# Kernel optimization log

Hardware: AMD Instinct MI355X
Metric: run time of the kernel (lower is better)

Reference implementation:

```python
import jax, jax.numpy as jnp
import numpy as np

N, E, F_IN, C, L = 50000, 800000, 64, 128, 2  # nodes, edges, input feats, channels, EGNN layers


def layer_norm(x, g, b, eps=1e-5):
    m = jnp.mean(x, -1, keepdims=True)
    v = jnp.var(x, -1, keepdims=True)
    return (x - m) / jnp.sqrt(v + eps) * g + b


def setup_inputs() -> dict:
    key = jax.random.key(0)
    ks = jax.random.split(key, 12)
    w = lambda k, shape: jax.random.normal(k, shape, jnp.float32) * 0.02
    return dict(
        node_attr=jax.random.normal(ks[0], (N, F_IN), jnp.float32),
        xyz=jax.random.normal(ks[1], (N, 3), jnp.float32),
        src=jax.random.randint(ks[2], (E,), 0, N, jnp.int32),
        dst=jax.random.randint(ks[3], (E,), 0, N, jnp.int32),
        # initial_node_embedding: Linear -> LN -> GELU -> Linear -> LN -> GELU (dropout off in eval)
        W_in1=w(ks[4], (F_IN, C)), b_in1=jnp.zeros((C,), jnp.float32),
        g_in1=jnp.ones((C,), jnp.float32), be_in1=jnp.zeros((C,), jnp.float32),
        W_in2=w(ks[5], (C, C)), b_in2=jnp.zeros((C,), jnp.float32),
        g_in2=jnp.ones((C,), jnp.float32), be_in2=jnp.zeros((C,), jnp.float32),
        # per-layer EGNNConv params (edge_feat_size=0), stacked over L layers
        We1=w(ks[6], (L, 2 * C + 1, C)), be1=jnp.zeros((L, C), jnp.float32),
        We2=w(ks[7], (L, C, C)), be2=jnp.zeros((L, C), jnp.float32),
        Wn1=w(ks[8], (L, 2 * C, C)), bn1=jnp.zeros((L, C), jnp.float32),
        Wn2=w(ks[9], (L, C, C)), bn2=jnp.zeros((L, C), jnp.float32),
    )


def reference(node_attr, xyz, src, dst,
              W_in1, b_in1, g_in1, be_in1, W_in2, b_in2, g_in2, be_in2,
              We1, be1, We2, be2, Wn1, bn1, Wn2, bn2):
    # initial node embedding (eval mode: dropout = identity; do_dropout=False)
    h = jax.nn.gelu(layer_norm(node_attr @ W_in1 + b_in1, g_in1, be_in1), approximate=False)
    h = jax.nn.gelu(layer_norm(h @ W_in2 + b_in2, g_in2, be_in2), approximate=False)

    # geometry is recomputed from the SAME xyz every layer (GraphConv passes the
    # original coord_feat to each EGNNConv and discards the updated coords)
    x_diff = xyz[src] - xyz[dst]                        # [E, 3]
    radial = jnp.sum(x_diff * x_diff, -1, keepdims=True)  # [E, 1]

    for l in range(L):
        f = jnp.concatenate([h[src], h[dst], radial], -1)  # [E, 2C+1]
        msg = jax.nn.silu(f @ We1[l] + be1[l])
        msg = jax.nn.silu(msg @ We2[l] + be2[l])            # [E, C]
        h_neigh = jax.ops.segment_sum(msg, dst, num_segments=N)  # sum to destination
        h = jax.nn.silu(jnp.concatenate([h, h_neigh], -1) @ Wn1[l] + bn1[l]) @ Wn2[l] + bn2[l]
    return h
```

## Files before the change

kernel.cpp:

```cpp
#include <hip/hip_runtime.h>
#include <stdint.h>

#define NND 50000
#define NED 800000
#define CH  128

typedef unsigned short us;
typedef unsigned int u32;
using bf16x8 = __attribute__((ext_vector_type(8))) __bf16;
using f32x4  = __attribute__((ext_vector_type(4))) float;

static __device__ __forceinline__ us f2bfu(float f){
  __bf16 b = (__bf16)f;
  return __builtin_bit_cast(us, b);
}
static __device__ __forceinline__ float silu_f(float x){
  return __fdividef(x, 1.0f + __expf(-x));
}
static __device__ __forceinline__ f32x4 mfma16(bf16x8 a, bf16x8 b, f32x4 c){
  return __builtin_amdgcn_mfma_f32_16x16x32_bf16(a, b, c, 0, 0, 0);
}
static __device__ __forceinline__ bf16x8 ldb8(const us* p){
  return *reinterpret_cast<const bf16x8*>(p);
}
static __device__ __forceinline__ float gelu_f(float x){
  return 0.5f*x*(1.0f + erff(x*0.70710678118654752f));
}

__global__ void prep_kernel(const float* __restrict__ We1, const float* __restrict__ We2,
                            const float* __restrict__ Wn1, const float* __restrict__ Wn2,
                            const float* __restrict__ Wi1, const float* __restrict__ Wi2,
                            us* __restrict__ We1T, us* __restrict__ We2T,
                            us* __restrict__ Wn1T, us* __restrict__ Wn2T,
                            us* __restrict__ Wi1T, us* __restrict__ Wi2T,
                            float* __restrict__ rw)
{
  int i = blockIdx.x * 256 + threadIdx.x;
  {
    int l = i >> 15, j = (i >> 8) & 127, k = i & 255;
    We1T[i] = f2bfu(We1[(l*257 + k)*128 + j]);
    Wn1T[i] = f2bfu(Wn1[(l*256 + k)*128 + j]);
  }
  if (i < 32768) {
    int l = i >> 14, j = (i >> 7) & 127, k = i & 127;
    We2T[i] = f2bfu(We2[(l*128 + k)*128 + j]);
    Wn2T[i] = f2bfu(Wn2[(l*128 + k)*128 + j]);
  }
  if (i < 8192) {
    int j = i >> 6, k = i & 63;
    Wi1T[i] = f2bfu(Wi1[k*128 + j]);
  }
  if (i < 16384) {
    int j = i >> 7, k = i & 127;
    Wi2T[i] = f2bfu(Wi2[k*128 + j]);
  }
  if (i < 256) {
    int l = i >> 7, j = i & 127;
    rw[i] = We1[(l*257 + 256)*128 + j];
  }
}

__global__ void hist_kernel(const int* __restrict__ dst, u32* __restrict__ counts)
{
  int e = blockIdx.x * 256 + threadIdx.x;
  if (e < NED) atomicAdd(&counts[dst[e]], 1u);
}

__global__ __launch_bounds__(1024, 1)
void scan_kernel(const u32* __restrict__ counts, u32* __restrict__ cursor)
{
  __shared__ u32 psum[1024];
  const int t = threadIdx.x;
  const int base = t * 49;
  u32 s = 0;
  u32 local[49];
  #pragma unroll 7
  for (int i = 0; i < 49; i++){
    int idx = base + i;
    u32 v = (idx < NND) ? counts[idx] : 0u;
    local[i] = v; s += v;
  }
  psum[t] = s; __syncthreads();
  for (int off = 1; off < 1024; off <<= 1){
    u32 v = (t >= off) ? psum[t - off] : 0u;
    __syncthreads();
    psum[t] += v;
    __syncthreads();
  }
  u32 run = psum[t] - s;
  #pragma unroll 7
  for (int i = 0; i < 49; i++){
    int idx = base + i;
    if (idx < NND) cursor[idx] = run;
    run += local[i];
  }
}

__global__ void scatter_kernel(const int* __restrict__ src, const int* __restrict__ dst,
                               const float* __restrict__ xyz, u32* __restrict__ cursor,
                               int* __restrict__ src_s, int* __restrict__ dst_s,
                               float* __restrict__ rad_s)
{
  int e = blockIdx.x * 256 + threadIdx.x;
  if (e >= NED) return;
  int s = src[e], d = dst[e];
  u32 p = atomicAdd(&cursor[d], 1u);
  float dx = xyz[3*s+0] - xyz[3*d+0];
  float dy = xyz[3*s+1] - xyz[3*d+1];
  float dz = xyz[3*s+2] - xyz[3*d+2];
  src_s[p] = s;
  dst_s[p] = d;
  rad_s[p] = dx*dx + dy*dy + dz*dz;
}

__global__ __launch_bounds__(256, 2)
void embed_kernel(const float* __restrict__ X,
                  const us* __restrict__ W1T, const float* __restrict__ b1,
                  const float* __restrict__ g1, const float* __restrict__ e1,
                  const us* __restrict__ W2T, const float* __restrict__ b2,
                  const float* __restrict__ g2, const float* __restrict__ e2,
                  us* __restrict__ hb)
{
  __shared__ __align__(16) us lds_all[4*16*136];
  const int tid = threadIdx.x;
  const int wid = tid >> 6, lane = tid & 63;
  const int c = lane & 15, g = lane >> 4;
  const int tile = blockIdx.x*4 + wid;
  if (tile >= 3125) return;
  us* lds = lds_all + wid * 2176;
  const int nb = tile * 16;

  const float* xrow = X + (size_t)(nb + c)*64;
  bf16x8 a1[2];
  #pragma unroll
  for (int ks = 0; ks < 2; ks++){
    const int kl = ks*32 + 8*g;
    f32x4 f0 = *reinterpret_cast<const f32x4*>(xrow + kl);
    f32x4 f1 = *reinterpret_cast<const f32x4*>(xrow + kl + 4);
    bf16x8 a;
    #pragma unroll
    for (int j = 0; j < 4; j++){ a[j] = (__bf16)f0[j]; a[4+j] = (__bf16)f1[j]; }
    a1[ks] = a;
  }

  f32x4 acc[8];
  #pragma unroll
  for (int t = 0; t < 8; t++){
    float bv = b1[16*t + c];
    #pragma unroll
    for (int r = 0; r < 4; r++) acc[t][r] = bv;
  }
  const us* brow1 = W1T + c*64;
  #pragma unroll
  for (int ks = 0; ks < 2; ks++){
    const int kl = ks*32 + 8*g;
    #pragma unroll
    for (int t = 0; t < 8; t++){
      bf16x8 b = ldb8(brow1 + t*16*64 + kl);
      acc[t] = mfma16(a1[ks], b, acc[t]);
    }
  }

  #pragma unroll
  for (int r = 0; r < 4; r++){
    float s = 0.0f, q = 0.0f;
    #pragma unroll
    for (int t = 0; t < 8; t++){ s += acc[t][r]; q += acc[t][r]*acc[t][r]; }
    #pragma unroll
    for (int off = 1; off < 16; off <<= 1){ s += __shfl_xor(s, off); q += __shfl_xor(q, off); }
    float mean = s * (1.0f/128.0f);
    float var  = q * (1.0f/128.0f) - mean*mean;
    float inv  = rsqrtf(var + 1e-5f);
    #pragma unroll
    for (int t = 0; t < 8; t++){
      float xn = (acc[t][r] - mean)*inv*g1[16*t+c] + e1[16*t+c];
      acc[t][r] = gelu_f(xn);
    }
  }

  #pragma unroll
  for (int t = 0; t < 8; t++)
    #pragma unroll
    for (int r = 0; r < 4; r++)
      lds[(4*g+r)*136 + 16*t + c] = f2bfu(acc[t][r]);

  asm volatile("s_waitcnt lgkmcnt(0)" ::: "memory");

  f32x4 acc2[8];
  #pragma unroll
  for (int t = 0; t < 8; t++){
    float bv = b2[16*t + c];
    #pragma unroll
    for (int r = 0; r < 4; r++) acc2[t][r] = bv;
  }
  const us* brow2 = W2T + c*128;
  #pragma unroll
  for (int ks = 0; ks < 4; ks++){
    const int kl = ks*32 + 8*g;
    bf16x8 a = *reinterpret_cast<const bf16x8*>(lds + c*136 + kl);
    #pragma unroll
    for (int t = 0; t < 8; t++){
      bf16x8 b = ldb8(brow2 + t*16*128 + kl);
      acc2[t] = mfma16(a, b, acc2[t]);
    }
  }

  #pragma unroll
  for (int r = 0; r < 4; r++){
    float s = 0.0f, q = 0.0f;
    #pragma unroll
    for (int t = 0; t < 8; t++){ s += acc2[t][r]; q += acc2[t][r]*acc2[t][r]; }
    #pragma unroll
    for (int off = 1; off < 16; off <<= 1){ s += __shfl_xor(s, off); q += __shfl_xor(q, off); }
    float mean = s * (1.0f/128.0f);
    float var  = q * (1.0f/128.0f) - mean*mean;
    float inv  = rsqrtf(var + 1e-5f);
    #pragma unroll
    for (int t = 0; t < 8; t++){
      float xn = (acc2[t][r] - mean)*inv*g2[16*t+c] + e2[16*t+c];
      float y  = gelu_f(xn);
      hb[(size_t)(nb + 4*g + r)*CH + 16*t + c] = f2bfu(y);
    }
  }
}

__global__ __launch_bounds__(256, 4)
void pq_kernel(const us* __restrict__ h, const us* __restrict__ W1T,
               const float* __restrict__ b1,
               us* __restrict__ P, us* __restrict__ Qb)
{
  const int tid = threadIdx.x;
  const int wid = tid >> 6, lane = tid & 63;
  const int c = lane & 15, g = lane >> 4;
  const int tile = blockIdx.x*4 + wid;
  if (tile >= 3125) return;
  const int nb = tile * 16;
  const us* arow = h + (size_t)(nb + c)*CH;

  bf16x8 a[4];
  #pragma unroll
  for (int ks = 0; ks < 4; ks++) a[ks] = ldb8(arow + ks*32 + 8*g);

  f32x4 accP[8], accQ[8];
  #pragma unroll
  for (int t = 0; t < 8; t++){
    float bq = b1[16*t + c];
    #pragma unroll
    for (int r = 0; r < 4; r++){ accP[t][r] = 0.0f; accQ[t][r] = bq; }
  }

  const us* brow = W1T + c*256;
  #pragma unroll
  for (int ks = 0; ks < 4; ks++){
    const int kl = ks*32 + 8*g;
    #pragma unroll
    for (int t = 0; t < 8; t++){
      bf16x8 bt = ldb8(brow + t*16*256 + kl);
      bf16x8 bb = ldb8(brow + t*16*256 + 128 + kl);
      accP[t] = mfma16(a[ks], bt, accP[t]);
      accQ[t] = mfma16(a[ks], bb, accQ[t]);
    }
  }

  #pragma unroll
  for (int t = 0; t < 8; t++)
    #pragma unroll
    for (int r = 0; r < 4; r++){
      size_t o = (size_t)(nb + 4*g + r)*CH + 16*t + c;
      P[o]  = f2bfu(accP[t][r]);
      Qb[o] = f2bfu(accQ[t][r]);
    }
}

__global__ __launch_bounds__(256, 2)
void edge_kernel(const us* __restrict__ P, const us* __restrict__ Qb,
                 const float* __restrict__ radial,
                 const int* __restrict__ src, const int* __restrict__ dst,
                 const float* __restrict__ rw,
                 const us* __restrict__ W2T, const float* __restrict__ b2,
                 float* __restrict__ hn)
{
  const int tid = threadIdx.x;
  const int wid = tid >> 6, lane = tid & 63;
  const int c = lane & 15, g = lane >> 4;
  const int eb = blockIdx.x * 128 + wid * 32;

  int sA[2], dA[2]; float radA[2];
  #pragma unroll
  for (int m = 0; m < 2; m++){
    int e = eb + m*16 + c;
    sA[m] = src[e]; dA[m] = dst[e]; radA[m] = radial[e];
  }
  int dste[2][4]; int dnxt[2];
  #pragma unroll
  for (int m = 0; m < 2; m++){
    #pragma unroll
    for (int r = 0; r < 4; r++) dste[m][r] = dst[eb + m*16 + 4*g + r];
    dnxt[m] = (g < 3) ? dst[eb + m*16 + 4*g + 4] : -1;
  }

  float rwf[4][8];
  #pragma unroll
  for (int ks = 0; ks < 4; ks++){
    f32x4 r0 = *reinterpret_cast<const f32x4*>(rw + ks*32 + 8*g);
    f32x4 r1 = *reinterpret_cast<const f32x4*>(rw + ks*32 + 8*g + 4);
    #pragma unroll
    for (int j = 0; j < 4; j++){ rwf[ks][j] = r0[j]; rwf[ks][4+j] = r1[j]; }
  }

  bf16x8 afrag[2][4];
  #pragma unroll
  for (int m = 0; m < 2; m++){
    const us* Pr = P  + (size_t)sA[m]*CH;
    const us* Qr = Qb + (size_t)dA[m]*CH;
    const float rv = radA[m];
    #pragma unroll
    for (int ks = 0; ks < 4; ks++){
      const int kl = ks*32 + 8*g;
      bf16x8 pv = ldb8(Pr + kl);
      bf16x8 qv = ldb8(Qr + kl);
      bf16x8 a;
      #pragma unroll
      for (int j = 0; j < 8; j++){
        float x = (float)pv[j] + (float)qv[j] + rv*rwf[ks][j];
        a[j] = (__bf16)silu_f(x);
      }
      afrag[m][ks] = a;
    }
  }

  float b2v[8];
  #pragma unroll
  for (int t = 0; t < 8; t++) b2v[t] = b2[16*t+c];
  f32x4 acc2[2][8];
  #pragma unroll
  for (int m = 0; m < 2; m++)
    #pragma unroll
    for (int t = 0; t < 8; t++)
      #pragma unroll
      for (int r = 0; r < 4; r++)
        acc2[m][t][r] = b2v[t];

  const us* brow2 = W2T + c*128;
  #pragma unroll
  for (int ks = 0; ks < 4; ks++){
    const int kl = ks*32 + 8*g;
    bf16x8 a0 = afrag[0][ks];
    bf16x8 a1 = afrag[1][ks];
    #pragma unroll
    for (int t = 0; t < 8; t++){
      bf16x8 b = ldb8(brow2 + t*16*128 + kl);
      acc2[0][t] = mfma16(a0, b, acc2[0][t]);
      acc2[1][t] = mfma16(a1, b, acc2[1][t]);
    }
  }

  #pragma unroll
  for (int m = 0; m < 2; m++){
    const int d0 = dste[m][0], d1 = dste[m][1], d2 = dste[m][2], d3 = dste[m][3];
    const int dn = dnxt[m];
    const bool eq01 = (d0 == d1), eq12 = (d1 == d2), eq23 = (d2 == d3);
    const bool chain = eq01 && eq12 && eq23;
    const int pd3 = __shfl_up(d3, 16);
    const bool cont = (pd3 == d0);
    #pragma unroll
    for (int t = 0; t < 8; t++){
      float v0 = silu_f(acc2[m][t][0]);
      float v1 = silu_f(acc2[m][t][1]);
      float v2 = silu_f(acc2[m][t][2]);
      float v3 = silu_f(acc2[m][t][3]);
      v1 += eq01 ? v0 : 0.0f;
      v2 += eq12 ? v1 : 0.0f;
      v3 += eq23 ? v2 : 0.0f;
      float cin = 0.0f;
      float v3a = v3;
      #pragma unroll
      for (int s = 1; s <= 3; s++){
        float pv = __shfl_up(v3a, 16);
        cin = (g == s && cont) ? pv : cin;
        v3a = v3 + (chain ? cin : 0.0f);
      }
      const int col = 16*t + c;
      float c1 = eq01 ? cin : 0.0f;
      float c2 = (eq01 && eq12) ? cin : 0.0f;
      if (!eq01)    unsafeAtomicAdd(&hn[(size_t)d0*CH + col], v0 + cin);
      if (!eq12)    unsafeAtomicAdd(&hn[(size_t)d1*CH + col], v1 + c1);
      if (!eq23)    unsafeAtomicAdd(&hn[(size_t)d2*CH + col], v2 + c2);
      if (d3 != dn) unsafeAtomicAdd(&hn[(size_t)d3*CH + col], v3a);
    }
  }
}

__global__ __launch_bounds__(256, 4)
void node_kernel(const us* __restrict__ h, const float* __restrict__ hn,
                 const us* __restrict__ W1T, const float* __restrict__ b1,
                 const us* __restrict__ W2T, const float* __restrict__ b2,
                 float* __restrict__ hout, us* __restrict__ hb)
{
  __shared__ __align__(16) us lds_all[4*16*136];
  const int tid = threadIdx.x;
  const int wid = tid >> 6, lane = tid & 63;
  const int c = lane & 15, g = lane >> 4;
  const int tile = blockIdx.x*4 + wid;
  if (tile >= 3125) return;
  us* lds = lds_all + wid * 2176;
  const int nb = tile * 16;
  const us*    arow = h  + (size_t)(nb + c)*CH;
  const float* nrow = hn + (size_t)(nb + c)*CH;

  float b1v[8];
  #pragma unroll
  for (int t = 0; t < 8; t++) b1v[t] = b1[16*t+c];
  f32x4 acc[8];
  #pragma unroll
  for (int t = 0; t < 8; t++)
    #pragma unroll
    for (int r = 0; r < 4; r++) acc[t][r] = b1v[t];

  const us* brow1 = W1T + c*256;
  #pragma unroll
  for (int ks = 0; ks < 8; ks++){
    const int kl = ks*32 + 8*g;
    bf16x8 a;
    if (ks < 4){
      a = ldb8(arow + kl);
    } else {
      const float* fp = nrow + (kl - 128);
      f32x4 f0 = *reinterpret_cast<const f32x4*>(fp);
      f32x4 f1 = *reinterpret_cast<const f32x4*>(fp + 4);
      #pragma unroll
      for (int i = 0; i < 4; i++){ a[i] = (__bf16)f0[i]; a[4+i] = (__bf16)f1[i]; }
    }
    #pragma unroll
    for (int t = 0; t < 8; t++){
      bf16x8 b = ldb8(brow1 + t*16*256 + kl);
      acc[t] = mfma16(a, b, acc[t]);
    }
  }

  #pragma unroll
  for (int t = 0; t < 8; t++)
    #pragma unroll
    for (int r = 0; r < 4; r++)
      lds[(4*g+r)*136 + 16*t + c] = f2bfu(silu_f(acc[t][r]));

  asm volatile("s_waitcnt lgkmcnt(0)" ::: "memory");

  float b2v[8];
  #pragma unroll
  for (int t = 0; t < 8; t++) b2v[t] = b2[16*t+c];
  f32x4 acc2[8];
  #pragma unroll
  for (int t = 0; t < 8; t++)
    #pragma unroll
    for (int r = 0; r < 4; r++) acc2[t][r] = b2v[t];

  const us* brow2 = W2T + c*128;
  #pragma unroll
  for (int ks = 0; ks < 4; ks++){
    const int kl = ks*32 + 8*g;
    bf16x8 a = *reinterpret_cast<const bf16x8*>(lds + c*136 + kl);
    #pragma unroll
    for (int t = 0; t < 8; t++){
      bf16x8 b = ldb8(brow2 + t*16*128 + kl);
      acc2[t] = mfma16(a, b, acc2[t]);
    }
  }

  #pragma unroll
  for (int t = 0; t < 8; t++)
    #pragma unroll
    for (int r = 0; r < 4; r++){
      int node = nb + 4*g + r;
      int col  = 16*t + c;
      float v  = acc2[t][r];
      if (hout) hout[(size_t)node*CH + col] = v;
      hb[(size_t)node*CH + col] = f2bfu(v);
    }
}

extern "C" void kernel_launch(void* const* d_in, const int* in_sizes, int n_in,
                              void* d_out, int out_size, void* d_ws, size_t ws_size,
                              hipStream_t stream)
{
  const float* X      = (const float*)d_in[0];
  const float* xyz    = (const float*)d_in[1];
  const int*   src    = (const int*)  d_in[2];
  const int*   dst    = (const int*)  d_in[3];
  const float* W_in1  = (const float*)d_in[4];
  const float* b_in1  = (const float*)d_in[5];
  const float* g_in1  = (const float*)d_in[6];
  const float* be_in1 = (const float*)d_in[7];
  const float* W_in2  = (const float*)d_in[8];
  const float* b_in2  = (const float*)d_in[9];
  const float* g_in2  = (const float*)d_in[10];
  const float* be_in2 = (const float*)d_in[11];
  const float* We1    = (const float*)d_in[12];
  const float* be1    = (const float*)d_in[13];
  const float* We2    = (const float*)d_in[14];
  const float* be2    = (const float*)d_in[15];
  const float* Wn1    = (const float*)d_in[16];
  const float* bn1    = (const float*)d_in[17];
  const float* Wn2    = (const float*)d_in[18];
  const float* bn2    = (const float*)d_in[19];

  char* ws = (char*)d_ws;
  us*    h_bf  = (us*)ws;    ws += (size_t)NND*CH*2;
  float* hn    = (float*)ws; ws += (size_t)NND*CH*4;
  us*    Pbuf  = (us*)ws;    ws += (size_t)NND*CH*2;
  us*    Qbuf  = (us*)ws;    ws += (size_t)NND*CH*2;
  float* rad_s = (float*)ws; ws += (size_t)NED*4;
  int*   src_s = (int*)ws;   ws += (size_t)NED*4;
  int*   dst_s = (int*)ws;   ws += (size_t)NED*4;
  us*    We1T  = (us*)ws;    ws += 2*128*256*2;
  us*    We2T  = (us*)ws;    ws += 2*128*128*2;
  us*    Wn1T  = (us*)ws;    ws += 2*128*256*2;
  us*    Wn2T  = (us*)ws;    ws += 2*128*128*2;
  us*    Wi1T  = (us*)ws;    ws += 128*64*2;
  us*    Wi2T  = (us*)ws;    ws += 128*128*2;
  float* rw    = (float*)ws; ws += 2*128*4;
  float* hout  = (float*)d_out;
  u32* counts = (u32*)hn;
  u32* cursor = (u32*)hn + NND;

  prep_kernel<<<256, 256, 0, stream>>>(We1, We2, Wn1, Wn2, W_in1, W_in2,
                                       We1T, We2T, Wn1T, Wn2T, Wi1T, Wi2T, rw);
  hipMemsetAsync(counts, 0, NND*sizeof(u32), stream);
  hist_kernel<<<3125, 256, 0, stream>>>(dst, counts);
  scan_kernel<<<1, 1024, 0, stream>>>(counts, cursor);
  scatter_kernel<<<3125, 256, 0, stream>>>(src, dst, xyz, cursor, src_s, dst_s, rad_s);
  embed_kernel<<<782, 256, 0, stream>>>(X, Wi1T, b_in1, g_in1, be_in1,
                                        Wi2T, b_in2, g_in2, be_in2, h_bf);
  for (int l = 0; l < 2; l++){
    pq_kernel<<<782, 256, 0, stream>>>(h_bf, We1T + l*128*256, be1 + l*128, Pbuf, Qbuf);
    hipMemsetAsync(hn, 0, (size_t)NND*CH*4, stream);
    edge_kernel<<<6250, 256, 0, stream>>>(Pbuf, Qbuf, rad_s, src_s, dst_s,
        rw + l*128, We2T + l*128*128, be2 + l*128, hn);
    node_kernel<<<782, 256, 0, stream>>>(h_bf, hn,
        Wn1T + l*128*256, bn1 + l*128,
        Wn2T + l*128*128, bn2 + l*128,
        (l == 1) ? hout : nullptr, h_bf);
  }
}
```

Before: 721.2 us.

## Parallelize CSR scan, remap edge blocks per XCD, skip final bf16 store

Replaces the single-block serial prefix scan over destination counts with a three-stage scan (per-wave sums, one top-level block scan, per-wave final scan), so the sort preparation is spread across many CUs. The edge kernel remaps block IDs so that each XCD processes a contiguous range of dst-sorted edges, which should improve L2 locality for scatter targets and gathered rows. The last node layer no longer writes the unused bf16 copy of h. This adds two kernel launches in exchange for less serial work.

```diff
diff --git a/kernel.cpp b/kernel.cpp
--- a/kernel.cpp
+++ b/kernel.cpp
@@ -4,6 +4,7 @@
 #define NND 50000
 #define NED 800000
 #define CH  128
+#define NCHUNK 782
 
 typedef unsigned short us;
 typedef unsigned int u32;
@@ -66,34 +67,48 @@
   if (e < NED) atomicAdd(&counts[dst[e]], 1u);
 }
 
+__global__ void scan_part_kernel(const u32* __restrict__ counts, u32* __restrict__ partial)
+{
+  const int w = blockIdx.x*4 + (threadIdx.x >> 6);
+  const int lane = threadIdx.x & 63;
+  const int idx = w*64 + lane;
+  u32 v = (idx < NND) ? counts[idx] : 0u;
+  #pragma unroll
+  for (int off = 1; off < 64; off <<= 1) v += __shfl_xor(v, off);
+  if (lane == 0 && w < NCHUNK) partial[w] = v;
+}
+
 __global__ __launch_bounds__(1024, 1)
-void scan_kernel(const u32* __restrict__ counts, u32* __restrict__ cursor)
-{
-  __shared__ u32 psum[1024];
+void scan_top_kernel(const u32* __restrict__ partial, u32* __restrict__ chunkoff)
+{
+  __shared__ u32 sh[1024];
   const int t = threadIdx.x;
-  const int base = t * 49;
-  u32 s = 0;
-  u32 local[49];
-  #pragma unroll 7
-  for (int i = 0; i < 49; i++){
-    int idx = base + i;
-    u32 v = (idx < NND) ? counts[idx] : 0u;
-    local[i] = v; s += v;
-  }
-  psum[t] = s; __syncthreads();
+  u32 p = (t < NCHUNK) ? partial[t] : 0u;
+  sh[t] = p; __syncthreads();
   for (int off = 1; off < 1024; off <<= 1){
-    u32 v = (t >= off) ? psum[t - off] : 0u;
+    u32 v = (t >= off) ? sh[t - off] : 0u;
     __syncthreads();
-    psum[t] += v;
+    sh[t] += v;
     __syncthreads();
   }
-  u32 run = psum[t] - s;
-  #pragma unroll 7
-  for (int i = 0; i < 49; i++){
-    int idx = base + i;
-    if (idx < NND) cursor[idx] = run;
-    run += local[i];
-  }
+  chunkoff[t] = sh[t] - p;
+}
+
+__global__ void scan_final_kernel(const u32* __restrict__ counts,
+                                  const u32* __restrict__ chunkoff,
+                                  u32* __restrict__ cursor)
+{
+  const int w = blockIdx.x*4 + (threadIdx.x >> 6);
+  const int lane = threadIdx.x & 63;
+  const int idx = w*64 + lane;
+  u32 v = (idx < NND) ? counts[idx] : 0u;
+  u32 x = v;
+  #pragma unroll
+  for (int off = 1; off < 64; off <<= 1){
+    u32 y = __shfl_up(x, off);
+    if (lane >= off) x += y;
+  }
+  if (idx < NND) cursor[idx] = x - v + chunkoff[w];
 }
 
 __global__ void scatter_kernel(const int* __restrict__ src, const int* __restrict__ dst,
@@ -283,7 +298,10 @@
   const int tid = threadIdx.x;
   const int wid = tid >> 6, lane = tid & 63;
   const int c = lane & 15, g = lane >> 4;
-  const int eb = blockIdx.x * 128 + wid * 32;
+  const int orig = blockIdx.x;
+  const int xcd = orig & 7, idx8 = orig >> 3;
+  const int blk = ((xcd < 2) ? xcd*782 : 2*782 + (xcd-2)*781) + idx8;
+  const int eb = blk * 128 + wid * 32;
 
   int sA[2], dA[2]; float radA[2];
   #pragma unroll
@@ -475,7 +493,7 @@
       int col  = 16*t + c;
       float v  = acc2[t][r];
       if (hout) hout[(size_t)node*CH + col] = v;
-      hb[(size_t)node*CH + col] = f2bfu(v);
+      if (hb)   hb[(size_t)node*CH + col] = f2bfu(v);
     }
 }
 
@@ -520,14 +538,18 @@
   us*    Wi2T  = (us*)ws;    ws += 128*128*2;
   float* rw    = (float*)ws; ws += 2*128*4;
   float* hout  = (float*)d_out;
-  u32* counts = (u32*)hn;
-  u32* cursor = (u32*)hn + NND;
+  u32* counts   = (u32*)hn;
+  u32* cursor   = (u32*)hn + NND;
+  u32* partial  = (u32*)hn + 2*NND;
+  u32* chunkoff = (u32*)hn + 2*NND + 1024;
 
   prep_kernel<<<256, 256, 0, stream>>>(We1, We2, Wn1, Wn2, W_in1, W_in2,
                                        We1T, We2T, Wn1T, Wn2T, Wi1T, Wi2T, rw);
   hipMemsetAsync(counts, 0, NND*sizeof(u32), stream);
   hist_kernel<<<3125, 256, 0, stream>>>(dst, counts);
-  scan_kernel<<<1, 1024, 0, stream>>>(counts, cursor);
+  scan_part_kernel<<<196, 256, 0, stream>>>(counts, partial);
+  scan_top_kernel<<<1, 1024, 0, stream>>>(partial, chunkoff);
+  scan_final_kernel<<<196, 256, 0, stream>>>(counts, chunkoff, cursor);
   scatter_kernel<<<3125, 256, 0, stream>>>(src, dst, xyz, cursor, src_s, dst_s, rad_s);
   embed_kernel<<<782, 256, 0, stream>>>(X, Wi1T, b_in1, g_in1, be_in1,
                                         Wi2T, b_in2, g_in2, be_in2, h_bf);
@@ -539,6 +561,6 @@
     node_kernel<<<782, 256, 0, stream>>>(h_bf, hn,
         Wn1T + l*128*256, bn1 + l*128,
         Wn2T + l*128*128, bn2 + l*128,
-        (l == 1) ? hout : nullptr, h_bf);
-  }
-}
+        (l == 1) ? hout : nullptr, (l == 0) ? h_bf : nullptr);
+  }
+}
```

Measured after the change: 636.7 us. -11.7%, faster.
